# Performance work log

Measured on AMD Instinct MI355X. Metric: run time of the kernel, lower is better.

## Reference

```python
import jax, jax.numpy as jnp
import numpy as np

# OGB/PyG molecular featurization vocab sizes (x_map / e_map)
NODE_VOCABS = [119, 9, 11, 12, 10, 5, 8, 2, 2]   # 9 atom features
EDGE_VOCABS = [22, 6, 2]                          # 3 bond features
HID, OUT, LAYERS = 128, 256, 3
N_NODES, N_EDGES, N_GRAPHS = 200000, 400000, 8000
NODE_OFF = np.concatenate([[0], np.cumsum(NODE_VOCABS)[:-1]]).astype(np.int32)
EDGE_OFF = np.concatenate([[0], np.cumsum(EDGE_VOCABS)[:-1]]).astype(np.int32)
NODE_TOT = int(np.sum(NODE_VOCABS))
EDGE_TOT = int(np.sum(EDGE_VOCABS))


def setup_inputs() -> dict:
    key = jax.random.key(0)
    ks = jax.random.split(key, 16)
    # integer graph data (values in-range per categorical column via modulo)
    x = jax.random.randint(ks[0], (N_NODES, 9), 0, 1 << 30) % jnp.asarray(NODE_VOCABS)
    edge_attr = jax.random.randint(ks[1], (N_EDGES, 3), 0, 1 << 30) % jnp.asarray(EDGE_VOCABS)
    edge_index = jax.random.randint(ks[2], (2, N_EDGES), 0, N_NODES)
    batch = jnp.sort(jax.random.randint(ks[3], (N_NODES,), 0, N_GRAPHS))
    s = 0.02
    return {
        "x": x, "edge_attr": edge_attr, "edge_index": edge_index, "batch": batch,
        # embedding tables packed row-wise with per-feature offsets
        "node_emb": jax.random.normal(ks[4], (NODE_TOT, HID), jnp.float32) * s,
        "edge_emb": jax.random.normal(ks[5], (EDGE_TOT, HID), jnp.float32) * s,
        "node_proj_w": jax.random.normal(ks[6], (9 * HID, HID), jnp.float32) * s,
        "node_proj_b": jnp.zeros((HID,), jnp.float32),
        "edge_proj_w": jax.random.normal(ks[7], (3 * HID, HID), jnp.float32) * s,
        "edge_proj_b": jnp.zeros((HID,), jnp.float32),
        "mlp_w1": jax.random.normal(ks[8], (LAYERS, HID, HID), jnp.float32) * s,
        "mlp_b1": jnp.zeros((LAYERS, HID), jnp.float32),
        "mlp_w2": jax.random.normal(ks[9], (LAYERS, HID, HID), jnp.float32) * s,
        "mlp_b2": jnp.zeros((LAYERS, HID), jnp.float32),
        "proj_w": jax.random.normal(ks[10], (HID, OUT), jnp.float32) * s,
        "proj_b": jnp.zeros((OUT,), jnp.float32),
    }


def reference(x, edge_attr, edge_index, batch,
              node_emb, edge_emb,
              node_proj_w, node_proj_b, edge_proj_w, edge_proj_b,
              mlp_w1, mlp_b1, mlp_w2, mlp_b2, proj_w, proj_b):
    n = x.shape[0]
    e = edge_attr.shape[0]
    # embedding lookup per categorical column, concat, project -> [N, HID]
    nf = node_emb[x + jnp.asarray(NODE_OFF)].reshape(n, 9 * HID)
    h = nf @ node_proj_w + node_proj_b
    ef = edge_emb[edge_attr + jnp.asarray(EDGE_OFF)].reshape(e, 3 * HID)
    ef = ef @ edge_proj_w + edge_proj_b
    src, dst = edge_index[0], edge_index[1]
    for l in range(LAYERS):
        # GINEConv (eps=0): mlp(x + sum_{j->i} relu(x_j + e_ji)), then outer relu
        m = jax.nn.relu(h[src] + ef)                       # [E, HID] gather + fuse
        agg = jax.ops.segment_sum(m, dst, num_segments=N_NODES)
        z = h + agg
        z = jax.nn.relu(z @ mlp_w1[l] + mlp_b1[l]) @ mlp_w2[l] + mlp_b2[l]
        h = jax.nn.relu(z)
    g = jax.ops.segment_sum(h, batch, num_segments=N_GRAPHS)  # global_add_pool
    p = g @ proj_w + proj_b
    norm = jnp.maximum(jnp.linalg.norm(p, axis=-1, keepdims=True), 1e-12)
    return p / norm
```

## Files before the change

kernel.cpp:

```cpp
#include <hip/hip_runtime.h>
#include <hip/hip_bf16.h>

#define NN 200000
#define NE 400000
#define NG 8000
#define HID 128
#define OUTD 256
#define NODE_TOT 178
#define NCOMBO 264
#define SCAN_NB 196

typedef __attribute__((ext_vector_type(8))) short bfrag8;
typedef __attribute__((ext_vector_type(4))) short bfrag4;
typedef __attribute__((ext_vector_type(4))) float f32x4;
typedef unsigned short ushort_t;

__constant__ int c_noff[10] = {0,119,128,139,151,161,166,174,176,178};

__device__ __forceinline__ ushort_t f2bf(float f) {
  union { float f; unsigned u; } x; x.f = f;
  unsigned r = x.u + 0x7fffu + ((x.u >> 16) & 1u);
  return (ushort_t)(r >> 16);
}
__device__ __forceinline__ float bf2f(ushort_t u) {
  union { unsigned u; float f; } x; x.u = ((unsigned)u) << 16;
  return x.f;
}

__global__ __launch_bounds__(128) void setup_tables(
    const float* __restrict__ node_emb, const float* __restrict__ edge_emb,
    const float* __restrict__ npw, const float* __restrict__ npb,
    const float* __restrict__ epw, const float* __restrict__ epb,
    const float* __restrict__ w1, const float* __restrict__ w2,
    float* __restrict__ PN, unsigned* __restrict__ pe3b,
    ushort_t* __restrict__ pw)
{
  int b = blockIdx.x, tid = threadIdx.x;
  if (b < NODE_TOT) {
    int r = b, d = tid;
    int c = 0;
    while (r >= c_noff[c+1]) c++;
    float acc = (c == 0) ? npb[d] : 0.f;
    const float* er = node_emb + r*HID;
    const float* wb = npw + (size_t)(c*HID)*HID + d;
    for (int k = 0; k < HID; k++) acc += er[k] * wb[(size_t)k*HID];
    PN[r*HID + d] = acc;
  } else if (b < NODE_TOT + NCOMBO) {
    if (tid >= 64) return;
    int c = b - NODE_TOT, lane = tid;
    int a2 = c & 1, a1 = (c >> 1) % 6, a0 = (c >> 1) / 6;
    int row[3] = { a0, 22 + a1, 28 + a2 };
    float v0 = epb[lane*2], v1 = epb[lane*2 + 1];
    #pragma unroll
    for (int f = 0; f < 3; f++) {
      const float* er = edge_emb + row[f]*HID;
      const float* wb = epw + (size_t)(f*HID)*HID;
      for (int k = 0; k < HID; k++) {
        float e = er[k];
        v0 += e * wb[(size_t)k*HID + lane*2];
        v1 += e * wb[(size_t)k*HID + lane*2 + 1];
      }
    }
    pe3b[c*64 + lane] = (unsigned)f2bf(v0) | ((unsigned)f2bf(v1) << 16);
  } else {
    int t = (b - NODE_TOT - NCOMBO)*128 + tid;
    if (t < 6144) {
      int lane = t & 63, tile = (t >> 6) & 31, layer = t >> 11;
      int nt = tile >> 2, kt = tile & 3;
      int n  = nt*16 + (lane & 15);
      int k0 = kt*32 + ((lane >> 4) << 3);
      const float* src = w1 + (size_t)layer*HID*HID;
      ushort_t* dst = pw + (size_t)layer*32768 + (size_t)tile*512 + lane*8;
      #pragma unroll
      for (int j = 0; j < 8; j++) dst[j] = f2bf(src[(size_t)(k0+j)*HID + n]);
    } else {
      int t2 = t - 6144;
      int lane = t2 & 63, frag = (t2 >> 6) & 63, layer = t2 >> 12;
      int it = frag >> 3, kk = frag & 7;
      int i  = it*16 + (lane & 15);
      int k0 = kk*16 + ((lane >> 4) << 2);
      const float* src = w2 + (size_t)layer*HID*HID;
      ushort_t* dst = pw + (size_t)layer*32768 + 16384 + (size_t)frag*256 + lane*4;
      #pragma unroll
      for (int j = 0; j < 4; j++) dst[j] = f2bf(src[(size_t)(k0+j)*HID + i]);
    }
  }
}

__global__ __launch_bounds__(256) void node_embed(const int* __restrict__ x,
                                                  const float* __restrict__ PN,
                                                  ushort_t* __restrict__ h)
{
  int gid = blockIdx.x*256 + threadIdx.x;
  int i = gid >> 5, d0 = (gid & 31) << 2;
  const int* xr = x + i*9;
  f32x4 acc = {0.f, 0.f, 0.f, 0.f};
  #pragma unroll
  for (int c = 0; c < 9; c++)
    acc += *(const f32x4*)&PN[(c_noff[c] + xr[c])*HID + d0];
  uint2 pk;
  pk.x = (unsigned)f2bf(acc[0]) | ((unsigned)f2bf(acc[1]) << 16);
  pk.y = (unsigned)f2bf(acc[2]) | ((unsigned)f2bf(acc[3]) << 16);
  *(uint2*)&h[(size_t)i*HID + d0] = pk;
}

__global__ __launch_bounds__(256) void hist(const int* __restrict__ ei, int* __restrict__ deg) {
  int e = blockIdx.x*256 + threadIdx.x;
  if (e < NE) atomicAdd(&deg[ei[NE + e]], 1);
}

__global__ __launch_bounds__(256) void scan1(const int* __restrict__ deg,
                                             int* __restrict__ rowptr,
                                             int* __restrict__ bsum)
{
  __shared__ int sd[256];
  int b = blockIdx.x, t = threadIdx.x;
  int idx0 = b*1024 + t*4;
  int v[4]; int s = 0;
  #pragma unroll
  for (int j = 0; j < 4; j++) { int i = idx0 + j; v[j] = (i < NN) ? deg[i] : 0; s += v[j]; }
  sd[t] = s; __syncthreads();
  for (int off = 1; off < 256; off <<= 1) {
    int x = (t >= off) ? sd[t - off] : 0; __syncthreads();
    sd[t] += x; __syncthreads();
  }
  int run = (t > 0) ? sd[t-1] : 0;
  #pragma unroll
  for (int j = 0; j < 4; j++) { int i = idx0 + j; run += v[j]; if (i < NN) rowptr[i+1] = run; }
  if (t == 255) bsum[b] = sd[255];
}

__global__ __launch_bounds__(256) void scan2(int* __restrict__ bsum) {
  __shared__ int sd[256];
  int t = threadIdx.x;
  sd[t] = (t < SCAN_NB) ? bsum[t] : 0; __syncthreads();
  for (int off = 1; off < 256; off <<= 1) {
    int x = (t >= off) ? sd[t - off] : 0; __syncthreads();
    sd[t] += x; __syncthreads();
  }
  if (t < SCAN_NB) bsum[t] = sd[t];
}

__global__ __launch_bounds__(256) void scan3(int* __restrict__ rowptr,
                                             const int* __restrict__ bsum,
                                             int* __restrict__ cursor)
{
  int b = blockIdx.x, t = threadIdx.x;
  int add = (b > 0) ? bsum[b-1] : 0;
  if (b == 0 && t == 0) { rowptr[0] = 0; cursor[0] = 0; }
  int idx0 = b*1024 + t*4;
  #pragma unroll
  for (int j = 0; j < 4; j++) {
    int i = idx0 + j;
    if (i < NN) {
      int v = rowptr[i+1] + add;
      rowptr[i+1] = v;
      cursor[i+1] = v;
    }
  }
}

__global__ __launch_bounds__(256) void scatter_e(const int* __restrict__ ei,
                                                 const int* __restrict__ ea,
                                                 int* __restrict__ cursor,
                                                 unsigned* __restrict__ elist,
                                                 int* __restrict__ dloc)
{
  int e = blockIdx.x*256 + threadIdx.x;
  if (e >= NE) return;
  int src = ei[e], dst = ei[NE + e];
  const int* ar = ea + e*3;
  unsigned combo = (unsigned)((ar[0]*6 + ar[1])*2 + ar[2]);
  int pos = atomicAdd(&cursor[dst], 1);
  elist[pos] = (unsigned)src | (combo << 18);
  dloc[pos] = dst & 63;
}

template<bool LAST>
__global__ __launch_bounds__(256, 4) void gine_layer(
    const ushort_t* __restrict__ hin, ushort_t* __restrict__ hout,
    const int* __restrict__ rowptr, const unsigned* __restrict__ elist,
    const int* __restrict__ dloc,
    const unsigned* __restrict__ pe3b,
    const ushort_t* __restrict__ pw,
    const float* __restrict__ b1, const float* __restrict__ b2,
    const int* __restrict__ batch, float* __restrict__ gf)
{
  __shared__ ushort_t aggs[64*136];
  __shared__ int bids[64];
  int tid = threadIdx.x;
  int w = tid >> 6, lane = tid & 63;
  int q = lane >> 4;
  int rb = blockIdx.x*64 + w*16;
  const unsigned* h2 = (const unsigned*)hin;

  if (LAST && tid < 64) bids[tid] = batch[blockIdx.x*64 + tid];

  #pragma unroll
  for (int r = 0; r < 16; r++)
    ((unsigned*)&aggs[(w*16 + r)*136])[lane] = 0;

  int s = __builtin_amdgcn_readfirstlane(rowptr[rb]);
  int E = __builtin_amdgcn_readfirstlane(rowptr[rb + 16]);
  int cur = -1;
  float ax = 0.f, ay = 0.f;

  auto proc = [&](int dl, unsigned hv, unsigned tt) {
    int dlu = __builtin_amdgcn_readfirstlane(dl);
    if (dlu != cur) {
      if (cur >= 0)
        ((unsigned*)&aggs[cur*136])[lane] =
            (unsigned)f2bf(ax) | ((unsigned)f2bf(ay) << 16);
      cur = dlu; ax = 0.f; ay = 0.f;
    }
    ax += fmaxf(bf2f((ushort_t)(hv & 0xffff)) + bf2f((ushort_t)(tt & 0xffff)), 0.f);
    ay += fmaxf(bf2f((ushort_t)(hv >> 16)) + bf2f((ushort_t)(tt >> 16)), 0.f);
  };

  int j = s;
  for (; j + 11 < E; j += 12) {
    unsigned pk[12]; int dl[12]; unsigned hv[12], tt[12];
    #pragma unroll
    for (int k = 0; k < 12; k++) { pk[k] = elist[j+k]; dl[k] = dloc[j+k]; }
    #pragma unroll
    for (int k = 0; k < 12; k++) {
      hv[k] = h2[(size_t)(pk[k] & 0x3ffff)*64 + lane];
      tt[k] = pe3b[(pk[k] >> 18)*64 + lane];
    }
    #pragma unroll
    for (int k = 0; k < 12; k++) proc(dl[k], hv[k], tt[k]);
  }
  for (; j < E; ++j) {
    unsigned pk = elist[j];
    int dl = dloc[j];
    unsigned hv = h2[(size_t)(pk & 0x3ffff)*64 + lane];
    unsigned tt = pe3b[(pk >> 18)*64 + lane];
    proc(dl, hv, tt);
  }
  if (cur >= 0)
    ((unsigned*)&aggs[cur*136])[lane] =
        (unsigned)f2bf(ax) | ((unsigned)f2bf(ay) << 16);

  int n = rb + (lane & 15);
  int acol = q << 3;

  bfrag8 afr[4];
  #pragma unroll
  for (int kt = 0; kt < 4; kt++) {
    int c = kt*32 + acol;
    bfrag8 hfr = *(const bfrag8*)(hin + (size_t)n*HID + c);
    bfrag8 gfr = *(const bfrag8*)&aggs[(w*16 + (lane & 15))*136 + c];
    bfrag8 fr;
    #pragma unroll
    for (int j2 = 0; j2 < 8; j2++)
      fr[j2] = (short)f2bf(bf2f((ushort_t)hfr[j2]) + bf2f((ushort_t)gfr[j2]));
    afr[kt] = fr;
  }

  if (LAST) __syncthreads();

  const bfrag8* w1f = (const bfrag8*)pw;
  const bfrag4* w2f = (const bfrag4*)(pw + 16384);

  f32x4 acc1[8];
  #pragma unroll
  for (int nt = 0; nt < 8; nt++)
    acc1[nt] = *(const f32x4*)&b1[nt*16 + q*4];
  #pragma unroll
  for (int kt = 0; kt < 4; kt++)
    #pragma unroll
    for (int nt = 0; nt < 8; nt++)
      acc1[nt] = __builtin_amdgcn_mfma_f32_16x16x32_bf16(w1f[(nt*4+kt)*64 + lane], afr[kt], acc1[nt], 0, 0, 0);

  bfrag4 t4[8];
  #pragma unroll
  for (int kk = 0; kk < 8; kk++) {
    bfrag4 v;
    #pragma unroll
    for (int r = 0; r < 4; r++) v[r] = (short)f2bf(fmaxf(acc1[kk][r], 0.f));
    t4[kk] = v;
  }

  #pragma unroll
  for (int it = 0; it < 8; it++) {
    f32x4 acc2 = *(const f32x4*)&b2[it*16 + q*4];
    #pragma unroll
    for (int kk = 0; kk < 8; kk++)
      acc2 = __builtin_amdgcn_mfma_f32_16x16x16bf16_1k(w2f[(it*8+kk)*64 + lane], t4[kk], acc2, 0, 0, 0);
    uint2 pk;
    pk.x = (unsigned)f2bf(fmaxf(acc2[0], 0.f)) | ((unsigned)f2bf(fmaxf(acc2[1], 0.f)) << 16);
    pk.y = (unsigned)f2bf(fmaxf(acc2[2], 0.f)) | ((unsigned)f2bf(fmaxf(acc2[3], 0.f)) << 16);
    if (LAST) {
      *(uint2*)&aggs[(w*16 + (lane & 15))*136 + it*16 + q*4] = pk;
    } else {
      *(uint2*)&hout[(size_t)n*HID + it*16 + q*4] = pk;
    }
  }

  if (LAST) {
    __syncthreads();
    int d = tid & 127, rh = tid >> 7;
    float acc = 0.f;
    int curg = bids[rh*32];
    for (int r = 0; r < 32; r++) {
      int row = rh*32 + r;
      int g = bids[row];
      if (g != curg) {
        atomicAdd(&gf[(size_t)curg*HID + d], acc);
        acc = 0.f; curg = g;
      }
      acc += bf2f(aggs[row*136 + d]);
    }
    atomicAdd(&gf[(size_t)curg*HID + d], acc);
  }
}

__global__ __launch_bounds__(256) void final_proj(const float* __restrict__ gf,
                                                  const float* __restrict__ W,
                                                  const float* __restrict__ b,
                                                  float* __restrict__ out)
{
  __shared__ float gls[16*128];
  __shared__ float part[16][4];
  int tid = threadIdx.x;
  int gbase = blockIdx.x*16;
  for (int idx = tid; idx < 2048; idx += 256) gls[idx] = gf[(size_t)gbase*128 + idx];
  __syncthreads();
  float acc[16];
  #pragma unroll
  for (int g = 0; g < 16; g++) acc[g] = 0.f;
  for (int k = 0; k < 128; k++) {
    float wv = W[(size_t)k*256 + tid];
    #pragma unroll
    for (int g = 0; g < 16; g++) acc[g] += gls[g*128 + k] * wv;
  }
  float bj = b[tid];
  int wid = tid >> 6, lane = tid & 63;
  #pragma unroll
  for (int g = 0; g < 16; g++) {
    acc[g] += bj;
    float s = acc[g]*acc[g];
    #pragma unroll
    for (int off = 32; off > 0; off >>= 1) s += __shfl_xor(s, off, 64);
    if (lane == 0) part[g][wid] = s;
  }
  __syncthreads();
  #pragma unroll
  for (int g = 0; g < 16; g++) {
    float S = part[g][0] + part[g][1] + part[g][2] + part[g][3];
    float rn = 1.f / fmaxf(sqrtf(S), 1e-12f);
    out[(size_t)(gbase + g)*256 + tid] = acc[g]*rn;
  }
}

__global__ __launch_bounds__(256) void ws_diag(float* __restrict__ out, int n, float wsval) {
  int i = blockIdx.x*256 + threadIdx.x;
  if (i < n) out[i] = (i == 0) ? wsval : 0.f;
}

extern "C" void kernel_launch(void* const* d_in, const int* in_sizes, int n_in,
                              void* d_out, int out_size, void* d_ws, size_t ws_size,
                              hipStream_t stream)
{
  const int*   x     = (const int*)d_in[0];
  const int*   ea    = (const int*)d_in[1];
  const int*   ei    = (const int*)d_in[2];
  const int*   batch = (const int*)d_in[3];
  const float* nemb  = (const float*)d_in[4];
  const float* eemb  = (const float*)d_in[5];
  const float* npw   = (const float*)d_in[6];
  const float* npb   = (const float*)d_in[7];
  const float* epw   = (const float*)d_in[8];
  const float* epb   = (const float*)d_in[9];
  const float* w1    = (const float*)d_in[10];
  const float* b1    = (const float*)d_in[11];
  const float* w2    = (const float*)d_in[12];
  const float* b2    = (const float*)d_in[13];
  const float* pjw   = (const float*)d_in[14];
  const float* pjb   = (const float*)d_in[15];
  float* out = (float*)d_out;

  char* ws = (char*)d_ws;
  size_t off = 0;
  auto carve = [&](size_t bytes) -> char* {
    char* p = ws + off;
    off = (off + bytes + 255) & ~(size_t)255;
    return p;
  };
  float*    PN     = (float*)carve((size_t)NODE_TOT*HID*4);
  unsigned* PE3b   = (unsigned*)carve((size_t)NCOMBO*64*4);
  ushort_t* PW     = (ushort_t*)carve((size_t)3*32768*2);
  ushort_t* hA     = (ushort_t*)carve((size_t)NN*HID*2);
  ushort_t* hB     = (ushort_t*)carve((size_t)NN*HID*2);
  int*      deg    = (int*)carve((size_t)NN*4);
  float*    gf     = (float*)carve((size_t)NG*HID*4);
  int*      rowptr = (int*)carve((size_t)(NN+1)*4);
  int*      cursor = (int*)carve((size_t)(NN+1)*4);
  int*      bsum   = (int*)carve((size_t)SCAN_NB*4);
  unsigned* elist  = (unsigned*)carve((size_t)NE*4);
  int*      dlc    = (int*)carve((size_t)NE*4);

  if (off > ws_size) {
    ws_diag<<<(out_size + 255)/256, 256, 0, stream>>>(out, out_size, (float)ws_size);
    return;
  }

  setup_tables<<<NODE_TOT + NCOMBO + 144, 128, 0, stream>>>(
      nemb, eemb, npw, npb, epw, epb, w1, w2, PN, PE3b, PW);
  node_embed<<<(NN*32)/256, 256, 0, stream>>>(x, PN, hA);

  hipMemsetAsync(deg, 0, (size_t)NN*4 + (size_t)NG*HID*4, stream);
  hist<<<(NE + 255)/256, 256, 0, stream>>>(ei, deg);
  scan1<<<SCAN_NB, 256, 0, stream>>>(deg, rowptr, bsum);
  scan2<<<1, 256, 0, stream>>>(bsum);
  scan3<<<SCAN_NB, 256, 0, stream>>>(rowptr, bsum, cursor);
  scatter_e<<<(NE + 255)/256, 256, 0, stream>>>(ei, ea, cursor, elist, dlc);

  gine_layer<false><<<NN/64, 256, 0, stream>>>(hA, hB, rowptr, elist, dlc, PE3b,
                                               PW, b1, b2, batch, gf);
  gine_layer<false><<<NN/64, 256, 0, stream>>>(hB, hA, rowptr, elist, dlc, PE3b,
                                               PW + 32768, b1 + HID, b2 + HID, batch, gf);
  gine_layer<true><<<NN/64, 256, 0, stream>>>(hA, hB, rowptr, elist, dlc, PE3b,
                                              PW + 65536, b1 + 2*HID, b2 + 2*HID, batch, gf);

  final_proj<<<NG/16, 256, 0, stream>>>(gf, pjw, pjb, out);
}
```

Measured before the change: 446.4 us.

## Fuse setup with histogram, embed with scatter, and pack edge records

Merges the degree histogram into the table-setup kernel and the node embedding into the edge scatter kernel, which removes two launches and lets independent work share one grid. Edge source/combo and local destination are packed into a single 64-bit record, so the layer loop does one load per edge instead of two. The node embedding now computes 8 columns per thread instead of 4. The risk is that merged grids mix dissimilar block workloads, and the 64-bit records double the per-edge element size even though total bytes stay the same.

```diff
diff --git a/kernel.cpp b/kernel.cpp
--- a/kernel.cpp
+++ b/kernel.cpp
@@ -14,6 +14,7 @@
 typedef __attribute__((ext_vector_type(4))) short bfrag4;
 typedef __attribute__((ext_vector_type(4))) float f32x4;
 typedef unsigned short ushort_t;
+typedef unsigned long long u64;
 
 __constant__ int c_noff[10] = {0,119,128,139,151,161,166,174,176,178};
 
@@ -27,13 +28,14 @@
   return x.f;
 }
 
-__global__ __launch_bounds__(128) void setup_tables(
+__global__ __launch_bounds__(128) void setup_hist(
     const float* __restrict__ node_emb, const float* __restrict__ edge_emb,
     const float* __restrict__ npw, const float* __restrict__ npb,
     const float* __restrict__ epw, const float* __restrict__ epb,
     const float* __restrict__ w1, const float* __restrict__ w2,
+    const int* __restrict__ ei,
     float* __restrict__ PN, unsigned* __restrict__ pe3b,
-    ushort_t* __restrict__ pw)
+    ushort_t* __restrict__ pw, int* __restrict__ deg)
 {
   int b = blockIdx.x, tid = threadIdx.x;
   if (b < NODE_TOT) {
@@ -62,7 +64,7 @@
       }
     }
     pe3b[c*64 + lane] = (unsigned)f2bf(v0) | ((unsigned)f2bf(v1) << 16);
-  } else {
+  } else if (b < NODE_TOT + NCOMBO + 144) {
     int t = (b - NODE_TOT - NCOMBO)*128 + tid;
     if (t < 6144) {
       int lane = t & 63, tile = (t >> 6) & 31, layer = t >> 11;
@@ -84,29 +86,10 @@
       #pragma unroll
       for (int j = 0; j < 4; j++) dst[j] = f2bf(src[(size_t)(k0+j)*HID + i]);
     }
-  }
-}
-
-__global__ __launch_bounds__(256) void node_embed(const int* __restrict__ x,
-                                                  const float* __restrict__ PN,
-                                                  ushort_t* __restrict__ h)
-{
-  int gid = blockIdx.x*256 + threadIdx.x;
-  int i = gid >> 5, d0 = (gid & 31) << 2;
-  const int* xr = x + i*9;
-  f32x4 acc = {0.f, 0.f, 0.f, 0.f};
-  #pragma unroll
-  for (int c = 0; c < 9; c++)
-    acc += *(const f32x4*)&PN[(c_noff[c] + xr[c])*HID + d0];
-  uint2 pk;
-  pk.x = (unsigned)f2bf(acc[0]) | ((unsigned)f2bf(acc[1]) << 16);
-  pk.y = (unsigned)f2bf(acc[2]) | ((unsigned)f2bf(acc[3]) << 16);
-  *(uint2*)&h[(size_t)i*HID + d0] = pk;
-}
-
-__global__ __launch_bounds__(256) void hist(const int* __restrict__ ei, int* __restrict__ deg) {
-  int e = blockIdx.x*256 + threadIdx.x;
-  if (e < NE) atomicAdd(&deg[ei[NE + e]], 1);
+  } else {
+    int e = (b - NODE_TOT - NCOMBO - 144)*128 + tid;
+    atomicAdd(&deg[ei[NE + e]], 1);
+  }
 }
 
 __global__ __launch_bounds__(256) void scan1(const int* __restrict__ deg,
@@ -160,27 +143,44 @@
   }
 }
 
-__global__ __launch_bounds__(256) void scatter_e(const int* __restrict__ ei,
-                                                 const int* __restrict__ ea,
-                                                 int* __restrict__ cursor,
-                                                 unsigned* __restrict__ elist,
-                                                 int* __restrict__ dloc)
-{
-  int e = blockIdx.x*256 + threadIdx.x;
-  if (e >= NE) return;
-  int src = ei[e], dst = ei[NE + e];
-  const int* ar = ea + e*3;
-  unsigned combo = (unsigned)((ar[0]*6 + ar[1])*2 + ar[2]);
-  int pos = atomicAdd(&cursor[dst], 1);
-  elist[pos] = (unsigned)src | (combo << 18);
-  dloc[pos] = dst & 63;
+__global__ __launch_bounds__(256) void scatter_embed(
+    const int* __restrict__ ei, const int* __restrict__ ea,
+    int* __restrict__ cursor, u64* __restrict__ epack,
+    const int* __restrict__ x, const float* __restrict__ PN,
+    ushort_t* __restrict__ h)
+{
+  int b = blockIdx.x, tid = threadIdx.x;
+  if (b < 1563) {
+    int e = b*256 + tid;
+    if (e >= NE) return;
+    int src = ei[e], dst = ei[NE + e];
+    const int* ar = ea + e*3;
+    unsigned combo = (unsigned)((ar[0]*6 + ar[1])*2 + ar[2]);
+    int pos = atomicAdd(&cursor[dst], 1);
+    epack[pos] = (u64)((unsigned)src | (combo << 18)) | ((u64)(dst & 63) << 32);
+  } else {
+    int gid = (b - 1563)*256 + tid;
+    int i = gid >> 4, d0 = (gid & 15) << 3;
+    const int* xr = x + i*9;
+    f32x4 a0 = {0.f,0.f,0.f,0.f}, a1 = {0.f,0.f,0.f,0.f};
+    #pragma unroll
+    for (int c = 0; c < 9; c++) {
+      const f32x4* p = (const f32x4*)&PN[(c_noff[c] + xr[c])*HID + d0];
+      a0 += p[0]; a1 += p[1];
+    }
+    uint4 pk;
+    pk.x = (unsigned)f2bf(a0[0]) | ((unsigned)f2bf(a0[1]) << 16);
+    pk.y = (unsigned)f2bf(a0[2]) | ((unsigned)f2bf(a0[3]) << 16);
+    pk.z = (unsigned)f2bf(a1[0]) | ((unsigned)f2bf(a1[1]) << 16);
+    pk.w = (unsigned)f2bf(a1[2]) | ((unsigned)f2bf(a1[3]) << 16);
+    *(uint4*)&h[(size_t)i*HID + d0] = pk;
+  }
 }
 
 template<bool LAST>
 __global__ __launch_bounds__(256, 4) void gine_layer(
     const ushort_t* __restrict__ hin, ushort_t* __restrict__ hout,
-    const int* __restrict__ rowptr, const unsigned* __restrict__ elist,
-    const int* __restrict__ dloc,
+    const int* __restrict__ rowptr, const u64* __restrict__ epack,
     const unsigned* __restrict__ pe3b,
     const ushort_t* __restrict__ pw,
     const float* __restrict__ b1, const float* __restrict__ b2,
@@ -219,23 +219,24 @@
 
   int j = s;
   for (; j + 11 < E; j += 12) {
-    unsigned pk[12]; int dl[12]; unsigned hv[12], tt[12];
-    #pragma unroll
-    for (int k = 0; k < 12; k++) { pk[k] = elist[j+k]; dl[k] = dloc[j+k]; }
+    u64 ep[12]; unsigned hv[12], tt[12];
+    #pragma unroll
+    for (int k = 0; k < 12; k++) ep[k] = epack[j+k];
     #pragma unroll
     for (int k = 0; k < 12; k++) {
-      hv[k] = h2[(size_t)(pk[k] & 0x3ffff)*64 + lane];
-      tt[k] = pe3b[(pk[k] >> 18)*64 + lane];
-    }
-    #pragma unroll
-    for (int k = 0; k < 12; k++) proc(dl[k], hv[k], tt[k]);
+      unsigned pk = (unsigned)ep[k];
+      hv[k] = h2[(size_t)(pk & 0x3ffff)*64 + lane];
+      tt[k] = pe3b[(pk >> 18)*64 + lane];
+    }
+    #pragma unroll
+    for (int k = 0; k < 12; k++) proc((int)(ep[k] >> 32), hv[k], tt[k]);
   }
   for (; j < E; ++j) {
-    unsigned pk = elist[j];
-    int dl = dloc[j];
+    u64 ep = epack[j];
+    unsigned pk = (unsigned)ep;
     unsigned hv = h2[(size_t)(pk & 0x3ffff)*64 + lane];
     unsigned tt = pe3b[(pk >> 18)*64 + lane];
-    proc(dl, hv, tt);
+    proc((int)(ep >> 32), hv, tt);
   }
   if (cur >= 0)
     ((unsigned*)&aggs[cur*136])[lane] =
@@ -397,30 +398,26 @@
   int*      rowptr = (int*)carve((size_t)(NN+1)*4);
   int*      cursor = (int*)carve((size_t)(NN+1)*4);
   int*      bsum   = (int*)carve((size_t)SCAN_NB*4);
-  unsigned* elist  = (unsigned*)carve((size_t)NE*4);
-  int*      dlc    = (int*)carve((size_t)NE*4);
+  u64*      epack  = (u64*)carve((size_t)NE*8);
 
   if (off > ws_size) {
     ws_diag<<<(out_size + 255)/256, 256, 0, stream>>>(out, out_size, (float)ws_size);
     return;
   }
 
-  setup_tables<<<NODE_TOT + NCOMBO + 144, 128, 0, stream>>>(
-      nemb, eemb, npw, npb, epw, epb, w1, w2, PN, PE3b, PW);
-  node_embed<<<(NN*32)/256, 256, 0, stream>>>(x, PN, hA);
-
   hipMemsetAsync(deg, 0, (size_t)NN*4 + (size_t)NG*HID*4, stream);
-  hist<<<(NE + 255)/256, 256, 0, stream>>>(ei, deg);
+  setup_hist<<<NODE_TOT + NCOMBO + 144 + 3125, 128, 0, stream>>>(
+      nemb, eemb, npw, npb, epw, epb, w1, w2, ei, PN, PE3b, PW, deg);
   scan1<<<SCAN_NB, 256, 0, stream>>>(deg, rowptr, bsum);
   scan2<<<1, 256, 0, stream>>>(bsum);
   scan3<<<SCAN_NB, 256, 0, stream>>>(rowptr, bsum, cursor);
-  scatter_e<<<(NE + 255)/256, 256, 0, stream>>>(ei, ea, cursor, elist, dlc);
-
-  gine_layer<false><<<NN/64, 256, 0, stream>>>(hA, hB, rowptr, elist, dlc, PE3b,
+  scatter_embed<<<1563 + 12500, 256, 0, stream>>>(ei, ea, cursor, epack, x, PN, hA);
+
+  gine_layer<false><<<NN/64, 256, 0, stream>>>(hA, hB, rowptr, epack, PE3b,
                                                PW, b1, b2, batch, gf);
-  gine_layer<false><<<NN/64, 256, 0, stream>>>(hB, hA, rowptr, elist, dlc, PE3b,
+  gine_layer<false><<<NN/64, 256, 0, stream>>>(hB, hA, rowptr, epack, PE3b,
                                                PW + 32768, b1 + HID, b2 + HID, batch, gf);
-  gine_layer<true><<<NN/64, 256, 0, stream>>>(hA, hB, rowptr, elist, dlc, PE3b,
+  gine_layer<true><<<NN/64, 256, 0, stream>>>(hA, hB, rowptr, epack, PE3b,
                                               PW + 65536, b1 + 2*HID, b2 + 2*HID, batch, gf);
 
   final_proj<<<NG/16, 256, 0, stream>>>(gf, pjw, pjb, out);
```

New measurement: 431.0 us. 3.5% less time.
